# Kernel tuning notes

Measured on AMD Instinct MI355X. Metric: run time of the kernel, lower is better.

## Reference

```python
import jax, jax.numpy as jnp
import numpy as np

N_VERTS, N_RADIAL, N_ANGULAR, FEAT = 100000, 5, 8, 16
AMT_TEMPLATES, OUTPUT_DIM = 8, 32


def setup_inputs() -> dict:
    key = jax.random.key(0)
    k1, k2, k3, k4, k5, k6 = jax.random.split(key, 6)
    mesh_signal = jax.random.normal(k1, (N_VERTS, FEAT), dtype=jnp.float32)
    bary_weights = jax.random.uniform(k2, (N_VERTS, N_RADIAL, N_ANGULAR, 3), dtype=jnp.float32)
    interp_coeffs = jax.random.uniform(
        k3, (N_RADIAL, N_ANGULAR, N_RADIAL * N_ANGULAR), dtype=jnp.float32)
    template_weights = jax.random.normal(
        k4, (AMT_TEMPLATES, OUTPUT_DIM, FEAT), dtype=jnp.float32)
    bias = jax.random.normal(k5, (AMT_TEMPLATES, OUTPUT_DIM), dtype=jnp.float32)
    bary_indices = jax.random.randint(k6, (N_VERTS, N_RADIAL, N_ANGULAR, 3), 0, N_VERTS, dtype=jnp.int32)
    return {
        "mesh_signal": mesh_signal,
        "bary_weights": bary_weights,
        "interp_coeffs": interp_coeffs,
        "template_weights": template_weights,
        "bias": bias,
        "bary_indices": bary_indices,
    }


def reference(mesh_signal, bary_weights, interp_coeffs, template_weights, bias, bary_indices):
    n, R, A, _ = bary_indices.shape
    K = R * A
    # --- patch operator: barycentric gather + weighted interpolation ---
    gathered = mesh_signal[bary_indices]                         # (n, R, A, 3, F)
    interp = jnp.einsum('nrak,nrakf->nraf', bary_weights, gathered)  # (n, R, A, F)
    # --- prior: matvec with interpolation coefficients over flattened template ---
    flat = interp.reshape(n, K, -1)                              # (n, K, F)
    interp = jnp.einsum('nkf,rak->nraf', flat, interp_coeffs)    # (n, R, A, F)
    # --- fold: W @ X then reduce_sum over template-vertex axis. Since the
    # activation comes AFTER the reduce_sum, sum(W @ X, -1) == W @ sum(X, -1),
    # so we reduce first to avoid an (n, T, O, K) intermediate. ---
    s = interp.reshape(n, K, -1).sum(axis=1)                     # (n, F)
    pre = jnp.einsum('tof,nf->nto', template_weights, s) + bias  # (n, T, O)
    act = jax.nn.relu(pre)
    return act.sum(axis=1)                                       # (n, O)
```

## Files before the change

### kernel.cpp

```cpp
#include <hip/hip_runtime.h>

#define KK 40
#define M3 120
#define MM4 30
#define RCH 15
#define FEAT 16
#define NT 8
#define ODIM 32
#define VPB 64
#define BLOCK 512
#define SST 17

typedef unsigned int u32;
typedef unsigned short u16;
typedef float  f32x2 __attribute__((ext_vector_type(2)));
typedef float  f32x4 __attribute__((ext_vector_type(4)));
typedef int    i32x4 __attribute__((ext_vector_type(4)));
typedef u32    u32x4 __attribute__((ext_vector_type(4)));

__device__ __forceinline__ u16 f2bf_rne(float x) {
    u32 u = __float_as_uint(x);
    u32 r = (u + 0x7fffu + ((u >> 16) & 1u)) >> 16;
    return (u16)r;
}

__global__ void prep_kernel(const float* __restrict__ mesh, const float* __restrict__ ic,
                            u16* __restrict__ mbf, float* __restrict__ cs3, int total) {
    const int t = threadIdx.x;
    if (blockIdx.x == 0) {
        __shared__ float cs[KK];
        if (t < KK) {
            float s = 0.f;
            #pragma unroll
            for (int ra = 0; ra < KK; ++ra) s += ic[ra * KK + t];
            cs[t] = s;
        }
        __syncthreads();
        if (t < M3) cs3[t] = cs[t / 3];
        return;
    }
    const int i = (blockIdx.x - 1) * BLOCK + t;
    const int base = i * 8;
    if (base < total) {
        f32x4 a = __builtin_nontemporal_load((const f32x4*)(mesh + base));
        f32x4 b = __builtin_nontemporal_load((const f32x4*)(mesh + base + 4));
        u32x4 v;
        v.x = (u32)f2bf_rne(a.x) | ((u32)f2bf_rne(a.y) << 16);
        v.y = (u32)f2bf_rne(a.z) | ((u32)f2bf_rne(a.w) << 16);
        v.z = (u32)f2bf_rne(b.x) | ((u32)f2bf_rne(b.y) << 16);
        v.w = (u32)f2bf_rne(b.z) | ((u32)f2bf_rne(b.w) << 16);
        *(u32x4*)(mbf + base) = v;
    }
}

__device__ __forceinline__ void acc8(f32x2 acc2[4], const u32x4 g, const float s) {
    const f32x2 s2 = {s, s};
    f32x2 p;
    p.x = __uint_as_float(g.x << 16);
    p.y = __uint_as_float(g.x & 0xffff0000u);
    acc2[0] = __builtin_elementwise_fma(p, s2, acc2[0]);
    p.x = __uint_as_float(g.y << 16);
    p.y = __uint_as_float(g.y & 0xffff0000u);
    acc2[1] = __builtin_elementwise_fma(p, s2, acc2[1]);
    p.x = __uint_as_float(g.z << 16);
    p.y = __uint_as_float(g.z & 0xffff0000u);
    acc2[2] = __builtin_elementwise_fma(p, s2, acc2[2]);
    p.x = __uint_as_float(g.w << 16);
    p.y = __uint_as_float(g.w & 0xffff0000u);
    acc2[3] = __builtin_elementwise_fma(p, s2, acc2[3]);
}

__device__ __forceinline__ void issue4_sc0(const u32x4* p0, const u32x4* p1,
                                           const u32x4* p2, const u32x4* p3,
                                           u32x4& g0, u32x4& g1, u32x4& g2, u32x4& g3) {
    asm volatile(
        "global_load_dwordx4 %0, %4, off sc0\n\t"
        "global_load_dwordx4 %1, %5, off sc0\n\t"
        "global_load_dwordx4 %2, %6, off sc0\n\t"
        "global_load_dwordx4 %3, %7, off sc0"
        : "=&v"(g0), "=&v"(g1), "=&v"(g2), "=&v"(g3)
        : "v"(p0), "v"(p1), "v"(p2), "v"(p3)
        : "memory");
}

#define WAIT_VM4() do { asm volatile("s_waitcnt vmcnt(4)" ::: "memory"); \
                        __builtin_amdgcn_sched_barrier(0); } while (0)
#define WAIT_VM0() do { asm volatile("s_waitcnt vmcnt(0)" ::: "memory"); \
                        __builtin_amdgcn_sched_barrier(0); } while (0)

struct GBatch { u32x4 g0, g1, g2, g3; float w0, w1, w2, w3; };

__device__ __forceinline__ void prep_issue(GBatch& B,
                                           const f32x4* __restrict__ s_bw4,
                                           const i32x4* __restrict__ s_bi4,
                                           int row, int cbase, int jc, int q, int mc, int b,
                                           const u16* __restrict__ mbf) {
    const int s0 = 2 * b, s1 = 2 * b + 1;
    const bool v0 = (mc == 0) || (s0 < 7);
    const bool v1 = (mc == 0) || (s1 < 7);
    const f32x4 wq0 = s_bw4[row + cbase + (v0 ? s0 : 0)];
    const i32x4 iq0 = s_bi4[row + cbase + (v0 ? s0 : 0)];
    const f32x4 wq1 = s_bw4[row + cbase + (v1 ? s1 : 0)];
    const i32x4 iq1 = s_bi4[row + cbase + (v1 ? s1 : 0)];
    B.w0 = v0 ? (jc ? wq0.z : wq0.x) : 0.f;
    B.w1 = v0 ? (jc ? wq0.w : wq0.y) : 0.f;
    B.w2 = v1 ? (jc ? wq1.z : wq1.x) : 0.f;
    B.w3 = v1 ? (jc ? wq1.w : wq1.y) : 0.f;
    const int i0 = v0 ? (jc ? iq0.z : iq0.x) : 0;
    const int i1 = v0 ? (jc ? iq0.w : iq0.y) : 0;
    const int i2 = v1 ? (jc ? iq1.z : iq1.x) : 0;
    const int i3 = v1 ? (jc ? iq1.w : iq1.y) : 0;
    issue4_sc0((const u32x4*)(mbf + (size_t)i0 * FEAT) + q,
               (const u32x4*)(mbf + (size_t)i1 * FEAT) + q,
               (const u32x4*)(mbf + (size_t)i2 * FEAT) + q,
               (const u32x4*)(mbf + (size_t)i3 * FEAT) + q,
               B.g0, B.g1, B.g2, B.g3);
}

__device__ __forceinline__ void consume(f32x2 acc2[4], const GBatch& B) {
    acc8(acc2, B.g0, B.w0);
    acc8(acc2, B.g1, B.w1);
    acc8(acc2, B.g2, B.w2);
    acc8(acc2, B.g3, B.w3);
}

__global__ __launch_bounds__(BLOCK, 6) void conv_kernel(
    const u16*   __restrict__ mbf,
    const float* __restrict__ bw,
    const float* __restrict__ W,
    const float* __restrict__ bias,
    const int*   __restrict__ bi,
    const float* __restrict__ cs3,
    float*       __restrict__ out,
    int n)
{
    __shared__ f32x4 s_buf[VPB * SST * 2];
    __shared__ float s_sig[VPB][FEAT + 1];

    f32x4* s_bw4 = s_buf;
    i32x4* s_bi4 = (i32x4*)(s_buf + VPB * SST);
    float (*s_out)[ODIM + 1] = (float(*)[ODIM + 1])s_buf;

    const int tid = threadIdx.x;
    const int vg0 = blockIdx.x * VPB;

    const f32x4* bw4g  = (const f32x4*)bw;
    const i32x4* bi4g  = (const i32x4*)bi;
    const f32x4* cs34g = (const f32x4*)cs3;

    const int vloc = tid >> 3;
    const int jc   = (tid >> 2) & 1;
    const int mc   = (tid >> 1) & 1;
    const int q    = tid & 1;
    const int vg   = vg0 + vloc;

    f32x2 acc2[4];
    #pragma unroll
    for (int e = 0; e < 4; ++e) acc2[e] = (f32x2){0.f, 0.f};

    #pragma unroll
    for (int r = 0; r < 2; ++r) {
        if (r) __syncthreads();

        #pragma unroll
        for (int ii = 0; ii < 2; ++ii) {
            const int i = tid + ii * BLOCK;
            if (i < VPB * RCH) {
                const int v = i / RCH;
                const int c = i - v * RCH;
                if (vg0 + v < n) {
                    const int gchunk = (vg0 + v) * MM4 + r * RCH + c;
                    f32x4 wv = __builtin_nontemporal_load(bw4g + gchunk);
                    i32x4 iv = __builtin_nontemporal_load(bi4g + gchunk);
                    const f32x4 cc = cs34g[r * RCH + c];
                    wv.x *= cc.x; wv.y *= cc.y; wv.z *= cc.z; wv.w *= cc.w;
                    s_bw4[v * SST + c] = wv;
                    s_bi4[v * SST + c] = iv;
                }
            }
        }
        __syncthreads();

        if (vg < n) {
            const int row   = vloc * SST;
            const int cbase = mc ? 8 : 0;
            GBatch A, B, C, D;
            prep_issue(A, s_bw4, s_bi4, row, cbase, jc, q, mc, 0, mbf);
            prep_issue(B, s_bw4, s_bi4, row, cbase, jc, q, mc, 1, mbf);
            WAIT_VM4();
            consume(acc2, A);
            prep_issue(C, s_bw4, s_bi4, row, cbase, jc, q, mc, 2, mbf);
            WAIT_VM4();
            consume(acc2, B);
            prep_issue(D, s_bw4, s_bi4, row, cbase, jc, q, mc, 3, mbf);
            WAIT_VM4();
            consume(acc2, C);
            WAIT_VM0();
            consume(acc2, D);
        }
    }

    float a8[8] = { acc2[0].x, acc2[0].y, acc2[1].x, acc2[1].y,
                    acc2[2].x, acc2[2].y, acc2[3].x, acc2[3].y };
    #pragma unroll
    for (int e = 0; e < 8; ++e) a8[e] += __shfl_xor(a8[e], 4);
    #pragma unroll
    for (int e = 0; e < 8; ++e) a8[e] += __shfl_xor(a8[e], 2);

    if (jc == 0) {
        const f32x4 v = (mc == 0) ? (f32x4){a8[0], a8[1], a8[2], a8[3]}
                                  : (f32x4){a8[4], a8[5], a8[6], a8[7]};
        *(f32x4*)(&s_sig[vloc][q * 8 + mc * 4]) = v;
    }
    __syncthreads();

    {
        const int lane = tid & 63;
        const int wave = __builtin_amdgcn_readfirstlane(tid >> 6);

        float s[FEAT];
        #pragma unroll
        for (int f = 0; f < FEAT; ++f) s[f] = s_sig[lane][f];

        f32x2 oacc[2];
        oacc[0] = (f32x2){0.f, 0.f};
        oacc[1] = (f32x2){0.f, 0.f};
        const f32x2 zero2 = {0.f, 0.f};

        #pragma unroll 2
        for (int t = 0; t < NT; ++t) {
            #pragma unroll
            for (int op = 0; op < 2; ++op) {
                const int o0 = wave * 4 + op * 2;
                f32x2 pre = { bias[t * ODIM + o0], bias[t * ODIM + o0 + 1] };
                const float* w0 = W + ((size_t)t * ODIM + o0) * FEAT;
                const float* w1 = w0 + FEAT;
                #pragma unroll
                for (int f = 0; f < FEAT; ++f) {
                    const f32x2 wp = { w0[f], w1[f] };
                    const f32x2 sp = { s[f], s[f] };
                    pre = __builtin_elementwise_fma(wp, sp, pre);
                }
                oacc[op] += __builtin_elementwise_max(pre, zero2);
            }
        }

        *(f32x4*)(&s_out[lane][wave * 4]) =
            (f32x4){oacc[0].x, oacc[0].y, oacc[1].x, oacc[1].y};
    }
    __syncthreads();

    {
        const int v   = tid >> 3;
        const int oq  = tid & 7;
        const int vgo = vg0 + v;
        if (vgo < n) {
            const f32x4 val = { s_out[v][oq * 4 + 0], s_out[v][oq * 4 + 1],
                                s_out[v][oq * 4 + 2], s_out[v][oq * 4 + 3] };
            *(f32x4*)(out + (size_t)vgo * ODIM + oq * 4) = val;
        }
    }
}

extern "C" void kernel_launch(void* const* d_in, const int* in_sizes, int n_in,
                              void* d_out, int out_size, void* d_ws, size_t ws_size,
                              hipStream_t stream) {
    const float* mesh = (const float*)d_in[0];
    const float* bw   = (const float*)d_in[1];
    const float* ic   = (const float*)d_in[2];
    const float* W    = (const float*)d_in[3];
    const float* bias = (const float*)d_in[4];
    const int*   bi   = (const int*)d_in[5];
    float* out = (float*)d_out;

    const int n = in_sizes[0] / FEAT;
    const int total = n * FEAT;

    float* cs3 = (float*)d_ws;
    u16*   mbf = (u16*)((char*)d_ws + 512);

    const int cvt_blocks = (total / 8 + BLOCK - 1) / BLOCK;
    prep_kernel<<<cvt_blocks + 1, BLOCK, 0, stream>>>(mesh, ic, mbf, cs3, total);

    const int blocks = (n + VPB - 1) / VPB;
    conv_kernel<<<blocks, BLOCK, 0, stream>>>(mbf, bw, W, bias, bi, cs3, out, n);
}
```

Baseline: 89.13 us.

## Stage all 30 chunks at once and gather in batches of six

Stages all 30 weight/index chunks per vertex into shared memory in one pass instead of two rounds of 15. This drops one block barrier and the wasted padded gathers with zero weight. The gather pipeline now issues six bf16 row loads per batch instead of four, so more loads are in flight per wave. In exchange, the shared-memory footprint roughly doubles (row stride 31) and the launch bound falls from 6 to 4. Fewer blocks can be resident per CU, which may reduce latency hiding for this gather-bound kernel.

```diff
diff --git a/kernel.cpp b/kernel.cpp
--- a/kernel.cpp
+++ b/kernel.cpp
@@ -3,13 +3,12 @@
 #define KK 40
 #define M3 120
 #define MM4 30
-#define RCH 15
 #define FEAT 16
 #define NT 8
 #define ODIM 32
 #define VPB 64
 #define BLOCK 512
-#define SST 17
+#define SST 31
 
 typedef unsigned int u32;
 typedef unsigned short u16;
@@ -70,61 +69,69 @@
     acc2[3] = __builtin_elementwise_fma(p, s2, acc2[3]);
 }
 
-__device__ __forceinline__ void issue4_sc0(const u32x4* p0, const u32x4* p1,
+__device__ __forceinline__ void issue6_sc0(const u32x4* p0, const u32x4* p1,
                                            const u32x4* p2, const u32x4* p3,
-                                           u32x4& g0, u32x4& g1, u32x4& g2, u32x4& g3) {
+                                           const u32x4* p4, const u32x4* p5,
+                                           u32x4& g0, u32x4& g1, u32x4& g2,
+                                           u32x4& g3, u32x4& g4, u32x4& g5) {
     asm volatile(
-        "global_load_dwordx4 %0, %4, off sc0\n\t"
-        "global_load_dwordx4 %1, %5, off sc0\n\t"
-        "global_load_dwordx4 %2, %6, off sc0\n\t"
-        "global_load_dwordx4 %3, %7, off sc0"
-        : "=&v"(g0), "=&v"(g1), "=&v"(g2), "=&v"(g3)
-        : "v"(p0), "v"(p1), "v"(p2), "v"(p3)
+        "global_load_dwordx4 %0, %6, off sc0\n\t"
+        "global_load_dwordx4 %1, %7, off sc0\n\t"
+        "global_load_dwordx4 %2, %8, off sc0\n\t"
+        "global_load_dwordx4 %3, %9, off sc0\n\t"
+        "global_load_dwordx4 %4, %10, off sc0\n\t"
+        "global_load_dwordx4 %5, %11, off sc0"
+        : "=&v"(g0), "=&v"(g1), "=&v"(g2), "=&v"(g3), "=&v"(g4), "=&v"(g5)
+        : "v"(p0), "v"(p1), "v"(p2), "v"(p3), "v"(p4), "v"(p5)
         : "memory");
 }
 
-#define WAIT_VM4() do { asm volatile("s_waitcnt vmcnt(4)" ::: "memory"); \
+#define WAIT_VM6() do { asm volatile("s_waitcnt vmcnt(6)" ::: "memory"); \
                         __builtin_amdgcn_sched_barrier(0); } while (0)
 #define WAIT_VM0() do { asm volatile("s_waitcnt vmcnt(0)" ::: "memory"); \
                         __builtin_amdgcn_sched_barrier(0); } while (0)
 
-struct GBatch { u32x4 g0, g1, g2, g3; float w0, w1, w2, w3; };
-
-__device__ __forceinline__ void prep_issue(GBatch& B,
-                                           const f32x4* __restrict__ s_bw4,
-                                           const i32x4* __restrict__ s_bi4,
-                                           int row, int cbase, int jc, int q, int mc, int b,
-                                           const u16* __restrict__ mbf) {
-    const int s0 = 2 * b, s1 = 2 * b + 1;
-    const bool v0 = (mc == 0) || (s0 < 7);
-    const bool v1 = (mc == 0) || (s1 < 7);
-    const f32x4 wq0 = s_bw4[row + cbase + (v0 ? s0 : 0)];
-    const i32x4 iq0 = s_bi4[row + cbase + (v0 ? s0 : 0)];
-    const f32x4 wq1 = s_bw4[row + cbase + (v1 ? s1 : 0)];
-    const i32x4 iq1 = s_bi4[row + cbase + (v1 ? s1 : 0)];
-    B.w0 = v0 ? (jc ? wq0.z : wq0.x) : 0.f;
-    B.w1 = v0 ? (jc ? wq0.w : wq0.y) : 0.f;
-    B.w2 = v1 ? (jc ? wq1.z : wq1.x) : 0.f;
-    B.w3 = v1 ? (jc ? wq1.w : wq1.y) : 0.f;
-    const int i0 = v0 ? (jc ? iq0.z : iq0.x) : 0;
-    const int i1 = v0 ? (jc ? iq0.w : iq0.y) : 0;
-    const int i2 = v1 ? (jc ? iq1.z : iq1.x) : 0;
-    const int i3 = v1 ? (jc ? iq1.w : iq1.y) : 0;
-    issue4_sc0((const u32x4*)(mbf + (size_t)i0 * FEAT) + q,
+struct GB6 { u32x4 g0, g1, g2, g3, g4, g5; float w0, w1, w2, w3, w4, w5; };
+
+__device__ __forceinline__ void prep3(GB6& B,
+                                      const f32x4* __restrict__ s_bw4,
+                                      const i32x4* __restrict__ s_bi4,
+                                      int row, int cbeg, int jc, int q,
+                                      const u16* __restrict__ mbf) {
+    const f32x4 wqa = s_bw4[row + cbeg + 0];
+    const i32x4 iqa = s_bi4[row + cbeg + 0];
+    const f32x4 wqb = s_bw4[row + cbeg + 1];
+    const i32x4 iqb = s_bi4[row + cbeg + 1];
+    const f32x4 wqc = s_bw4[row + cbeg + 2];
+    const i32x4 iqc = s_bi4[row + cbeg + 2];
+    B.w0 = jc ? wqa.z : wqa.x;  B.w1 = jc ? wqa.w : wqa.y;
+    B.w2 = jc ? wqb.z : wqb.x;  B.w3 = jc ? wqb.w : wqb.y;
+    B.w4 = jc ? wqc.z : wqc.x;  B.w5 = jc ? wqc.w : wqc.y;
+    const int i0 = jc ? iqa.z : iqa.x;
+    const int i1 = jc ? iqa.w : iqa.y;
+    const int i2 = jc ? iqb.z : iqb.x;
+    const int i3 = jc ? iqb.w : iqb.y;
+    const int i4 = jc ? iqc.z : iqc.x;
+    const int i5 = jc ? iqc.w : iqc.y;
+    issue6_sc0((const u32x4*)(mbf + (size_t)i0 * FEAT) + q,
                (const u32x4*)(mbf + (size_t)i1 * FEAT) + q,
                (const u32x4*)(mbf + (size_t)i2 * FEAT) + q,
                (const u32x4*)(mbf + (size_t)i3 * FEAT) + q,
-               B.g0, B.g1, B.g2, B.g3);
-}
-
-__device__ __forceinline__ void consume(f32x2 acc2[4], const GBatch& B) {
+               (const u32x4*)(mbf + (size_t)i4 * FEAT) + q,
+               (const u32x4*)(mbf + (size_t)i5 * FEAT) + q,
+               B.g0, B.g1, B.g2, B.g3, B.g4, B.g5);
+}
+
+__device__ __forceinline__ void consume6(f32x2 acc2[4], const GB6& B) {
     acc8(acc2, B.g0, B.w0);
     acc8(acc2, B.g1, B.w1);
     acc8(acc2, B.g2, B.w2);
     acc8(acc2, B.g3, B.w3);
-}
-
-__global__ __launch_bounds__(BLOCK, 6) void conv_kernel(
+    acc8(acc2, B.g4, B.w4);
+    acc8(acc2, B.g5, B.w5);
+}
+
+__global__ __launch_bounds__(BLOCK, 4) void conv_kernel(
     const u16*   __restrict__ mbf,
     const float* __restrict__ bw,
     const float* __restrict__ W,
@@ -154,50 +161,48 @@
     const int q    = tid & 1;
     const int vg   = vg0 + vloc;
 
+    #pragma unroll
+    for (int ii = 0; ii < 4; ++ii) {
+        const int i = tid + ii * BLOCK;
+        if (i < VPB * MM4) {
+            const int v = i / MM4;
+            const int c = i - v * MM4;
+            if (vg0 + v < n) {
+                const int gchunk = (vg0 + v) * MM4 + c;
+                f32x4 wv = __builtin_nontemporal_load(bw4g + gchunk);
+                i32x4 iv = __builtin_nontemporal_load(bi4g + gchunk);
+                const f32x4 cc = cs34g[c];
+                wv.x *= cc.x; wv.y *= cc.y; wv.z *= cc.z; wv.w *= cc.w;
+                s_bw4[v * SST + c] = wv;
+                s_bi4[v * SST + c] = iv;
+            }
+        }
+    }
+    __syncthreads();
+
     f32x2 acc2[4];
     #pragma unroll
     for (int e = 0; e < 4; ++e) acc2[e] = (f32x2){0.f, 0.f};
 
-    #pragma unroll
-    for (int r = 0; r < 2; ++r) {
-        if (r) __syncthreads();
-
-        #pragma unroll
-        for (int ii = 0; ii < 2; ++ii) {
-            const int i = tid + ii * BLOCK;
-            if (i < VPB * RCH) {
-                const int v = i / RCH;
-                const int c = i - v * RCH;
-                if (vg0 + v < n) {
-                    const int gchunk = (vg0 + v) * MM4 + r * RCH + c;
-                    f32x4 wv = __builtin_nontemporal_load(bw4g + gchunk);
-                    i32x4 iv = __builtin_nontemporal_load(bi4g + gchunk);
-                    const f32x4 cc = cs34g[r * RCH + c];
-                    wv.x *= cc.x; wv.y *= cc.y; wv.z *= cc.z; wv.w *= cc.w;
-                    s_bw4[v * SST + c] = wv;
-                    s_bi4[v * SST + c] = iv;
-                }
-            }
-        }
-        __syncthreads();
-
-        if (vg < n) {
-            const int row   = vloc * SST;
-            const int cbase = mc ? 8 : 0;
-            GBatch A, B, C, D;
-            prep_issue(A, s_bw4, s_bi4, row, cbase, jc, q, mc, 0, mbf);
-            prep_issue(B, s_bw4, s_bi4, row, cbase, jc, q, mc, 1, mbf);
-            WAIT_VM4();
-            consume(acc2, A);
-            prep_issue(C, s_bw4, s_bi4, row, cbase, jc, q, mc, 2, mbf);
-            WAIT_VM4();
-            consume(acc2, B);
-            prep_issue(D, s_bw4, s_bi4, row, cbase, jc, q, mc, 3, mbf);
-            WAIT_VM4();
-            consume(acc2, C);
-            WAIT_VM0();
-            consume(acc2, D);
-        }
+    if (vg < n) {
+        const int row   = vloc * SST;
+        const int cbase = mc * 15;
+        GB6 A, B, C;
+        prep3(A, s_bw4, s_bi4, row, cbase + 0, jc, q, mbf);
+        prep3(B, s_bw4, s_bi4, row, cbase + 3, jc, q, mbf);
+        WAIT_VM6();
+        consume6(acc2, A);
+        prep3(C, s_bw4, s_bi4, row, cbase + 6, jc, q, mbf);
+        WAIT_VM6();
+        consume6(acc2, B);
+        prep3(A, s_bw4, s_bi4, row, cbase + 9, jc, q, mbf);
+        WAIT_VM6();
+        consume6(acc2, C);
+        prep3(B, s_bw4, s_bi4, row, cbase + 12, jc, q, mbf);
+        WAIT_VM6();
+        consume6(acc2, A);
+        WAIT_VM0();
+        consume6(acc2, B);
     }
 
     float a8[8] = { acc2[0].x, acc2[0].y, acc2[1].x, acc2[1].y,
```

Result: faster. 85.58 us (-4.0%).
